# Optimization experiments

Hardware: AMD Instinct MI355X
Metric: run time of the kernel (lower is better)

The kernel has to match this reference:

```python
import jax, jax.numpy as jnp
import numpy as np

MARGIN = 0.1

def setup_inputs() -> dict:
    key = jax.random.key(0)
    k1, k2 = jax.random.split(key)
    embeddings = jax.random.normal(k1, (8192, 128), dtype=jnp.float32)
    labels = jax.random.randint(k2, (8192,), 0, 64, dtype=jnp.int64)
    return {"embeddings": embeddings, "labels": labels}

def reference(embeddings, labels):
    # sim[i,j] = <e_i, e_j>
    sim = embeddings @ embeddings.T  # [n, n]
    eq = labels[:, None] == labels[None, :]  # pos mask (includes diagonal)
    # per entry: exp(margin - sim) for positives, exp(sim - margin) for negatives
    terms = jnp.where(eq, jnp.exp(MARGIN - sim), jnp.exp(sim - MARGIN))
    # loss_i = log(sum_j terms[i,j]); loss = mean_i loss_i
    return jnp.mean(jnp.log(jnp.sum(terms, axis=1)))
```

## Files before the change

### kernel.cpp

```cpp
#include <hip/hip_runtime.h>
#include <hip/hip_bf16.h>

#define N 8192
#define D 128
#define LOG2E  1.44269504088896f
#define LN2    0.69314718055995f
#define COLSB  272

typedef __attribute__((ext_vector_type(8))) short bf16x8;
typedef __attribute__((ext_vector_type(4))) float f32x4;

#if __has_builtin(__builtin_amdgcn_exp2f)
#define EXP2(x) __builtin_amdgcn_exp2f(x)
#else
#define EXP2(x) exp2f(x)
#endif
#if __has_builtin(__builtin_amdgcn_logf)
#define LOG2(x) __builtin_amdgcn_logf(x)
#else
#define LOG2(x) log2f(x)
#endif

static __device__ __forceinline__ unsigned short f2bf(float f) {
    union { float f; unsigned int u; } x;
    x.f = f;
    unsigned int r = ((x.u >> 16) & 1u) + 0x7FFFu;
    return (unsigned short)((x.u + r) >> 16);
}

__global__ void prep_kernel(const float* __restrict__ E,
                            unsigned short* __restrict__ Eb,
                            float* __restrict__ rowsum,
                            float* __restrict__ out) {
    int idx = blockIdx.x * 256 + threadIdx.x;
    float4 v = ((const float4*)E)[idx];
    ushort4 o;
    o.x = f2bf(v.x); o.y = f2bf(v.y); o.z = f2bf(v.z); o.w = f2bf(v.w);
    ((ushort4*)Eb)[idx] = o;
    if (idx < N) rowsum[idx] = 0.0f;
    if (idx == 0) out[0] = 0.0f;
}

__global__ __launch_bounds__(256) void fused_kernel(
        const unsigned short* __restrict__ Eb,
        const int* __restrict__ labels,
        float* __restrict__ rowsum) {
    __shared__ __align__(16) char bB[128 * COLSB];
    __shared__ int   labC[128];
    __shared__ int   labR[128];
    __shared__ float colacc[128];

    const int tid  = threadIdx.x;
    const int wid  = tid >> 6;
    const int lane = tid & 63;
    const int q = lane >> 4;
    const int l = lane & 15;

    const int b = blockIdx.x;
    int r = (int)(64.5f - sqrtf(64.5f * 64.5f - 2.0f * (float)b));
    while ((r + 1) * 64 - ((r + 1) * r) / 2 <= b) ++r;
    while (r * 64 - (r * (r - 1)) / 2 > b) --r;
    const int c = r + (b - (r * 64 - (r * (r - 1)) / 2));
    const bool diag = (r == c);
    const int tile_m0 = r * 128;
    const int n_begin = c * 128;
    const int mrow0 = tile_m0 + wid * 32;

    bf16x8 a[2][4];
#pragma unroll
    for (int g = 0; g < 2; ++g) {
        const bf16x8* p = (const bf16x8*)(Eb + (size_t)(mrow0 + g * 16 + l) * D + q * 8);
#pragma unroll
        for (int kk = 0; kk < 4; ++kk) a[g][kk] = p[kk * 4];
    }
    const char* gB = (const char*)Eb + (size_t)n_begin * 256;
    const int col  = tid >> 1;
    const int half = tid & 1;
    const float4* src = (const float4*)(gB + col * 256 + half * 128);
    float4 st[8];
#pragma unroll
    for (int i = 0; i < 8; ++i) st[i] = src[i];
    int labv = (tid < 128) ? labels[n_begin + tid]
                           : labels[tile_m0 + (tid - 128)];

    float4* dst = (float4*)(bB + col * COLSB + half * 128);
#pragma unroll
    for (int i = 0; i < 8; ++i) dst[i] = st[i];
    if (tid < 128) { labC[tid] = labv; colacc[tid] = 0.0f; }
    else           { labR[tid - 128] = labv; }
    __syncthreads();

    int lrow[8];
#pragma unroll
    for (int g = 0; g < 2; ++g)
#pragma unroll
        for (int rr = 0; rr < 4; ++rr)
            lrow[g * 4 + rr] = labR[wid * 32 + g * 16 + q * 4 + rr];

    float sum[8];
#pragma unroll
    for (int i = 0; i < 8; ++i) sum[i] = 0.0f;

#pragma clang loop unroll(disable)
    for (int s = 0; s < 8; ++s) {
        const int lc = labC[s * 16 + l];
        const char* lb = bB + (s * 16 + l) * COLSB + q * 16;
        bf16x8 b0 = *(const bf16x8*)(lb);
        bf16x8 b1 = *(const bf16x8*)(lb + 64);
        bf16x8 b2 = *(const bf16x8*)(lb + 128);
        bf16x8 b3 = *(const bf16x8*)(lb + 192);

        f32x4 acc0 = (f32x4){0.f, 0.f, 0.f, 0.f};
        f32x4 acc1 = (f32x4){0.f, 0.f, 0.f, 0.f};
        acc0 = __builtin_amdgcn_mfma_f32_16x16x32_bf16(a[0][0], b0, acc0, 0, 0, 0);
        acc0 = __builtin_amdgcn_mfma_f32_16x16x32_bf16(a[0][1], b1, acc0, 0, 0, 0);
        acc0 = __builtin_amdgcn_mfma_f32_16x16x32_bf16(a[0][2], b2, acc0, 0, 0, 0);
        acc0 = __builtin_amdgcn_mfma_f32_16x16x32_bf16(a[0][3], b3, acc0, 0, 0, 0);
        acc1 = __builtin_amdgcn_mfma_f32_16x16x32_bf16(a[1][0], b0, acc1, 0, 0, 0);
        acc1 = __builtin_amdgcn_mfma_f32_16x16x32_bf16(a[1][1], b1, acc1, 0, 0, 0);
        acc1 = __builtin_amdgcn_mfma_f32_16x16x32_bf16(a[1][2], b2, acc1, 0, 0, 0);
        acc1 = __builtin_amdgcn_mfma_f32_16x16x32_bf16(a[1][3], b3, acc1, 0, 0, 0);

        float cp = 0.0f;
#pragma unroll
        for (int g = 0; g < 2; ++g) {
#pragma unroll
            for (int rr = 0; rr < 4; ++rr) {
                float sv = (g == 0) ? acc0[rr] : acc1[rr];
                bool eq = (lrow[g * 4 + rr] == lc);
                float cc = eq ? -LOG2E : LOG2E;
                float term = EXP2(cc * (sv - 0.1f));
                sum[g * 4 + rr] += term;
                cp += term;
            }
        }
        if (!diag) {
            cp += __shfl_xor(cp, 16);
            cp += __shfl_xor(cp, 32);
            if (q == 0) atomicAdd(&colacc[s * 16 + l], cp);
        }
    }

#pragma unroll
    for (int i = 0; i < 8; ++i) {
        float v = sum[i];
        v += __shfl_xor(v, 1);
        v += __shfl_xor(v, 2);
        v += __shfl_xor(v, 4);
        v += __shfl_xor(v, 8);
        sum[i] = v;
    }
    if (l == 0) {
#pragma unroll
        for (int g = 0; g < 2; ++g)
#pragma unroll
            for (int rr = 0; rr < 4; ++rr)
                atomicAdd(&rowsum[mrow0 + g * 16 + q * 4 + rr], sum[g * 4 + rr]);
    }

    __syncthreads();
    if (!diag && tid < 128) atomicAdd(&rowsum[n_begin + tid], colacc[tid]);
}

__global__ void finalize_kernel(const float* __restrict__ rowsum, float* __restrict__ out) {
    __shared__ float red[4];
    int i = blockIdx.x * 256 + threadIdx.x;
    float v = LOG2(rowsum[i]) * LN2;
#pragma unroll
    for (int off = 1; off <= 32; off <<= 1) v += __shfl_xor(v, off);
    if ((threadIdx.x & 63) == 0) red[threadIdx.x >> 6] = v;
    __syncthreads();
    if (threadIdx.x == 0)
        atomicAdd(out, (red[0] + red[1] + red[2] + red[3]) * (1.0f / (float)N));
}

extern "C" void kernel_launch(void* const* d_in, const int* in_sizes, int n_in,
                              void* d_out, int out_size, void* d_ws, size_t ws_size,
                              hipStream_t stream) {
    const float* E = (const float*)d_in[0];
    const int* labels = (const int*)d_in[1];
    float* out = (float*)d_out;

    unsigned short* Eb = (unsigned short*)d_ws;
    float* rowsum = (float*)((char*)d_ws + (size_t)N * D * sizeof(unsigned short));

    prep_kernel<<<1024, 256, 0, stream>>>(E, Eb, rowsum, out);
    fused_kernel<<<2080, 256, 0, stream>>>(Eb, labels, rowsum);
    finalize_kernel<<<32, 256, 0, stream>>>(rowsum, out);
}
```

Before: 90.88 us.

## Replace global rowsum atomics with per-tile partial buffers reduced in finalize

The fused kernel now writes its row and column partial sums as plain stores into a [64 x N] partial buffer indexed by tile column or row, replacing the global float atomics. Finalize sums the 64 partials per row, and the last block, chosen by an atomic ticket counter, reduces the block results deterministically, so the rowsum zeroing is no longer needed. This removes atomic contention on rowsum and gives deterministic results, at the cost of extra memory traffic: 2 MB written and then read back in finalize.

```diff
diff --git a/kernel.cpp b/kernel.cpp
--- a/kernel.cpp
+++ b/kernel.cpp
@@ -30,21 +30,19 @@
 
 __global__ void prep_kernel(const float* __restrict__ E,
                             unsigned short* __restrict__ Eb,
-                            float* __restrict__ rowsum,
-                            float* __restrict__ out) {
+                            unsigned int* __restrict__ counter) {
     int idx = blockIdx.x * 256 + threadIdx.x;
     float4 v = ((const float4*)E)[idx];
     ushort4 o;
     o.x = f2bf(v.x); o.y = f2bf(v.y); o.z = f2bf(v.z); o.w = f2bf(v.w);
     ((ushort4*)Eb)[idx] = o;
-    if (idx < N) rowsum[idx] = 0.0f;
-    if (idx == 0) out[0] = 0.0f;
+    if (idx == 0) *counter = 0u;
 }
 
 __global__ __launch_bounds__(256) void fused_kernel(
         const unsigned short* __restrict__ Eb,
         const int* __restrict__ labels,
-        float* __restrict__ rowsum) {
+        float* __restrict__ part) {
     __shared__ __align__(16) char bB[128 * COLSB];
     __shared__ int   labC[128];
     __shared__ int   labR[128];
@@ -155,23 +153,49 @@
         for (int g = 0; g < 2; ++g)
 #pragma unroll
             for (int rr = 0; rr < 4; ++rr)
-                atomicAdd(&rowsum[mrow0 + g * 16 + q * 4 + rr], sum[g * 4 + rr]);
-    }
-
-    __syncthreads();
-    if (!diag && tid < 128) atomicAdd(&rowsum[n_begin + tid], colacc[tid]);
-}
-
-__global__ void finalize_kernel(const float* __restrict__ rowsum, float* __restrict__ out) {
+                part[(size_t)c * N + mrow0 + g * 16 + q * 4 + rr] = sum[g * 4 + rr];
+    }
+
+    __syncthreads();
+    if (!diag && tid < 128)
+        part[(size_t)r * N + n_begin + tid] = colacc[tid];
+}
+
+__global__ void finalize_kernel(const float* __restrict__ part,
+                                float* __restrict__ bpart,
+                                unsigned int* __restrict__ counter,
+                                float* __restrict__ out) {
     __shared__ float red[4];
-    int i = blockIdx.x * 256 + threadIdx.x;
-    float v = LOG2(rowsum[i]) * LN2;
+    __shared__ unsigned int tk;
+    const int tid = threadIdx.x;
+    const int i = blockIdx.x * 256 + tid;
+
+    float s = 0.0f;
+#pragma unroll 8
+    for (int x = 0; x < 64; ++x) s += part[(size_t)x * N + i];
+    float v = LOG2(s) * LN2;
 #pragma unroll
     for (int off = 1; off <= 32; off <<= 1) v += __shfl_xor(v, off);
-    if ((threadIdx.x & 63) == 0) red[threadIdx.x >> 6] = v;
-    __syncthreads();
-    if (threadIdx.x == 0)
-        atomicAdd(out, (red[0] + red[1] + red[2] + red[3]) * (1.0f / (float)N));
+    if ((tid & 63) == 0) red[tid >> 6] = v;
+    __syncthreads();
+    if (tid == 0) {
+        bpart[blockIdx.x] = red[0] + red[1] + red[2] + red[3];
+        __threadfence();
+        tk = atomicAdd(counter, 1u);
+    }
+    __syncthreads();
+    if (tk == 31u) {
+        __threadfence();
+        if (tid < 64) {
+            float t = (tid < 32)
+                ? __hip_atomic_load(&bpart[tid], __ATOMIC_RELAXED,
+                                    __HIP_MEMORY_SCOPE_AGENT)
+                : 0.0f;
+#pragma unroll
+            for (int off = 1; off <= 32; off <<= 1) t += __shfl_xor(t, off);
+            if (tid == 0) out[0] = t * (1.0f / (float)N);
+        }
+    }
 }
 
 extern "C" void kernel_launch(void* const* d_in, const int* in_sizes, int n_in,
@@ -182,9 +206,11 @@
     float* out = (float*)d_out;
 
     unsigned short* Eb = (unsigned short*)d_ws;
-    float* rowsum = (float*)((char*)d_ws + (size_t)N * D * sizeof(unsigned short));
-
-    prep_kernel<<<1024, 256, 0, stream>>>(E, Eb, rowsum, out);
-    fused_kernel<<<2080, 256, 0, stream>>>(Eb, labels, rowsum);
-    finalize_kernel<<<32, 256, 0, stream>>>(rowsum, out);
-}
+    float* part = (float*)((char*)d_ws + (size_t)N * D * 2);
+    float* bpart = part + (size_t)64 * N;
+    unsigned int* counter = (unsigned int*)(bpart + 32);
+
+    prep_kernel<<<1024, 256, 0, stream>>>(E, Eb, counter);
+    fused_kernel<<<2080, 256, 0, stream>>>(Eb, labels, part);
+    finalize_kernel<<<32, 256, 0, stream>>>(part, bpart, counter, out);
+}
```

Measured after the change: 90.03 us. Within noise of the previous version (-0.9%).
